# Optimization experiments

Measured on AMD Instinct MI355X. Metric: run time of the kernel, lower is better.

The kernel has to match this reference:

```python
import jax, jax.numpy as jnp
import numpy as np

B, T, D = 8, 2048, 128


def setup_inputs() -> dict:
    key = jax.random.key(0)
    kq, kk, kv = jax.random.split(key, 3)
    q = jax.random.normal(kq, (B, T, D), dtype=jnp.float32)
    k = jax.random.normal(kk, (B, T, D), dtype=jnp.float32)
    v = jax.random.normal(kv, (B, T, D), dtype=jnp.float32)
    # causal mask, broadcast over batch; 0 -> masked
    mask = jnp.tril(jnp.ones((T, T), dtype=jnp.int32))[None, :, :]
    mode = jnp.float32(0.5)  # learnable scalar parameter (init 0.5)
    return {"q": q, "k": k, "v": v, "mask": mask, "mode": mode}


def reference(q, k, v, mask, mode):
    scale = D ** (-0.5)
    # meson score: -(Q K^T) * scale
    meson = -jnp.einsum("btd,bsd->bts", q, k) * scale
    # baryon score: Q against K with feature dim rolled by 1
    k_perm = jnp.roll(k, shift=1, axis=-1)
    baryon = jnp.einsum("btd,bsd->bts", q, k_perm) * scale
    alpha = jax.nn.sigmoid(mode)
    attn = alpha * meson + (1.0 - alpha) * baryon
    attn = jnp.where(mask == 0, -jnp.inf, attn)
    attn = jax.nn.softmax(attn, axis=-1)
    return jnp.einsum("bts,bsd->btd", attn, v)
```

## Files before the change

### kernel.cpp

```cpp
#include <hip/hip_runtime.h>
#include <hip/hip_bf16.h>
#include <cstdint>
#include <cstddef>


typedef __attribute__((ext_vector_type(8))) short short8;
typedef __attribute__((ext_vector_type(4))) float f32x4;

#define T_DIM 2048
#define D_DIM 128
#define B_DIM 8
#define SEGT 4
#define POSLOTS_PER_B 56
#define MLSLOTS_PER_B 72

__device__ __forceinline__ unsigned short f2bf(float f) {
  unsigned u = __builtin_bit_cast(unsigned, f);
  u += 0x7FFFu + ((u >> 16) & 1u);
  return (unsigned short)(u >> 16);
}
__device__ __forceinline__ float bf2f(unsigned short u) {
  return __uint_as_float(((unsigned)u) << 16);
}
__device__ __forceinline__ void gload_lds16(const void* g, void* l) {
  __builtin_amdgcn_global_load_lds(
      (const __attribute__((address_space(1))) unsigned int*)g,
      (__attribute__((address_space(3))) unsigned int*)l, 16, 0, 0);
}

__global__ __launch_bounds__(256) void prep_all(
    const float* __restrict__ q, const float* __restrict__ k, const float* __restrict__ v,
    const float* __restrict__ modep,
    unsigned short* __restrict__ qbf, unsigned short* __restrict__ kbf,
    unsigned short* __restrict__ vt)
{
  __shared__ unsigned short tile[64 * 136];
  const int b = blockIdx.x, s0 = blockIdx.y * 64;
  const int tid = threadIdx.x;
  const float alpha = 1.f / (1.f + __expf(-modep[0]));
  const float scale = 0.08838834764831845f;
  const float ca = -alpha * scale, cb = (1.f - alpha) * scale;

#pragma unroll
  for (int u = 0; u < 4; ++u) {
    int c = u * 256 + tid;
    int r = c >> 4, c8 = c & 15;
    size_t row = (size_t)b * T_DIM + s0 + r;
    float4 ka = *(const float4*)(k + row * D_DIM + c8 * 8);
    float4 kb2 = *(const float4*)(k + row * D_DIM + c8 * 8 + 4);
    short8 ko = { (short)f2bf(ka.x), (short)f2bf(ka.y), (short)f2bf(ka.z), (short)f2bf(ka.w),
                  (short)f2bf(kb2.x), (short)f2bf(kb2.y), (short)f2bf(kb2.z), (short)f2bf(kb2.w) };
    *(short8*)(kbf + row * D_DIM + c8 * 8) = ko;
    const float* qr = q + row * D_DIM;
    float e[9];
    float4 f0 = *(const float4*)(qr + c8 * 8);
    float4 f1 = *(const float4*)(qr + c8 * 8 + 4);
    e[0] = f0.x; e[1] = f0.y; e[2] = f0.z; e[3] = f0.w;
    e[4] = f1.x; e[5] = f1.y; e[6] = f1.z; e[7] = f1.w;
    e[8] = qr[(c8 * 8 + 8) & 127];
    short8 qo;
#pragma unroll
    for (int j = 0; j < 8; ++j) qo[j] = (short)f2bf(ca * e[j] + cb * e[j + 1]);
    *(short8*)(qbf + row * D_DIM + c8 * 8) = qo;
    float4 va = *(const float4*)(v + row * D_DIM + c8 * 8);
    float4 vb2 = *(const float4*)(v + row * D_DIM + c8 * 8 + 4);
    short8 vo = { (short)f2bf(va.x), (short)f2bf(va.y), (short)f2bf(va.z), (short)f2bf(va.w),
                  (short)f2bf(vb2.x), (short)f2bf(vb2.y), (short)f2bf(vb2.z), (short)f2bf(vb2.w) };
    *(short8*)(tile + r * 136 + c8 * 8) = vo;
  }
  __syncthreads();
#pragma unroll
  for (int u = 0; u < 8; ++u) {
    int c = u * 256 + tid;
    int d = c >> 4, sq = c & 15;
    ushort4 o = { tile[(sq * 4 + 0) * 136 + d], tile[(sq * 4 + 1) * 136 + d],
                  tile[(sq * 4 + 2) * 136 + d], tile[(sq * 4 + 3) * 136 + d] };
    *(ushort4*)(vt + ((size_t)b * D_DIM + d) * T_DIM + s0 + sq * 4) = o;
  }
}

__global__ __launch_bounds__(256, 2) void attn_kernel(
    const unsigned short* __restrict__ qbf, const unsigned short* __restrict__ kbf,
    const unsigned short* __restrict__ vt, float* __restrict__ out,
    unsigned short* __restrict__ po, float* __restrict__ ml)
{
  __shared__ uint4 smem4[4608];
  char* smem = (char*)smem4;
  const int tid = threadIdx.x;
  const int w = tid >> 6, lane = tid & 63;
  const int t16 = lane & 15, g = lane >> 4;
  const int b = blockIdx.x;
  const int c = blockIdx.y;
  const int s = blockIdx.z;
  const int nt = 2 * c + 2;
  const int nseg = (c + 2) >> 1;
  if (s >= nseg) return;
  const int t0 = s * SEGT;
  const int t1 = min(nt, t0 + SEGT);
  const int qb = c * 128 + w * 32;

  char* pw = smem + 65536 + w * 2048;
  const unsigned short* kbase = kbf + (size_t)b * T_DIM * D_DIM;
  const unsigned short* vbase = vt + (size_t)b * D_DIM * T_DIM;

  short8 qf[2][4];
#pragma unroll
  for (int mt = 0; mt < 2; ++mt) {
    const unsigned short* qr = qbf + ((size_t)b * T_DIM + qb + mt * 16 + t16) * D_DIM + g * 8;
#pragma unroll
    for (int dd = 0; dd < 4; ++dd) qf[mt][dd] = *(const short8*)(qr + dd * 32);
  }

  f32x4 acc[2][8];
#pragma unroll
  for (int mt = 0; mt < 2; ++mt)
#pragma unroll
    for (int dt = 0; dt < 8; ++dt) acc[mt][dt] = (f32x4){0.f, 0.f, 0.f, 0.f};
  float mrun[2][4], lsum[2][4];
#pragma unroll
  for (int mt = 0; mt < 2; ++mt)
#pragma unroll
    for (int r = 0; r < 4; ++r) { mrun[mt][r] = -1e30f; lsum[mt][r] = 0.f; }

  auto stage = [&](int cur, int kt) {
    const int kv0 = kt * 64;
    char* kb = smem + cur * 16384;
    char* vb = smem + 32768 + cur * 16384;
#pragma unroll
    for (int u = 0; u < 4; ++u) {
      int s_loc = w * 16 + u * 4 + (lane >> 4);
      int slot = (lane & 15) ^ (s_loc & 7);
      gload_lds16(kbase + (size_t)(kv0 + s_loc) * D_DIM + slot * 8,
                  kb + w * 4096 + u * 1024);
    }
#pragma unroll
    for (int u = 0; u < 4; ++u) {
      int d_loc = w * 32 + u * 8 + (lane >> 3);
      int vslot = (lane & 7) ^ (d_loc & 7);
      gload_lds16(vbase + (size_t)d_loc * T_DIM + kv0 + vslot * 8,
                  vb + w * 4096 + u * 1024);
    }
  };

  stage(0, t0);
  __syncthreads();
  int cur = 0;

  for (int kt = t0; kt < t1; ++kt) {
    if (kt + 1 < t1) stage(cur ^ 1, kt + 1);
    const int kv0 = kt * 64;

    if (kv0 <= qb + 31) {
      char* kb = smem + cur * 16384;
      char* vb = smem + 32768 + cur * 16384;

      f32x4 sj[2][4];
#pragma unroll
      for (int jt = 0; jt < 4; ++jt) {
        int srow = jt * 16 + t16;
        int rb = srow * 256, swz = (srow & 7) << 4;
        f32x4 s0 = (f32x4){0.f, 0.f, 0.f, 0.f};
        f32x4 s1 = (f32x4){0.f, 0.f, 0.f, 0.f};
#pragma unroll
        for (int dd = 0; dd < 4; ++dd) {
          short8 kf = *(const short8*)(kb + ((rb + dd * 64 + g * 16) ^ swz));
          s0 = __builtin_amdgcn_mfma_f32_16x16x32_bf16(qf[0][dd], kf, s0, 0, 0, 0);
          s1 = __builtin_amdgcn_mfma_f32_16x16x32_bf16(qf[1][dd], kf, s1, 0, 0, 0);
        }
        sj[0][jt] = s0; sj[1][jt] = s1;
      }

      if (kv0 + 63 > qb) {
#pragma unroll
        for (int mt = 0; mt < 2; ++mt)
#pragma unroll
          for (int jt = 0; jt < 4; ++jt) {
            int sg = kv0 + jt * 16 + t16;
#pragma unroll
            for (int r = 0; r < 4; ++r) {
              int tg = qb + mt * 16 + 4 * g + r;
              if (sg > tg) sj[mt][jt][r] = -1e30f;
            }
          }
      }

      float lm[2][4];
      int ok = 1;
#pragma unroll
      for (int mt = 0; mt < 2; ++mt)
#pragma unroll
        for (int r = 0; r < 4; ++r) {
          lm[mt][r] = fmaxf(fmaxf(sj[mt][0][r], sj[mt][1][r]),
                            fmaxf(sj[mt][2][r], sj[mt][3][r]));
          ok &= (lm[mt][r] <= mrun[mt][r] + 8.0f);
        }
      if (!__all(ok)) {
#pragma unroll
        for (int mt = 0; mt < 2; ++mt) {
          float tm[4];
#pragma unroll
          for (int r = 0; r < 4; ++r) tm[r] = lm[mt][r];
#pragma unroll
          for (int r = 0; r < 4; ++r) {
            tm[r] = fmaxf(tm[r], __shfl_xor(tm[r], 1));
            tm[r] = fmaxf(tm[r], __shfl_xor(tm[r], 2));
            tm[r] = fmaxf(tm[r], __shfl_xor(tm[r], 4));
            tm[r] = fmaxf(tm[r], __shfl_xor(tm[r], 8));
          }
#pragma unroll
          for (int r = 0; r < 4; ++r) {
            float mnew = fmaxf(mrun[mt][r], tm[r]);
            float corr = __expf(mrun[mt][r] - mnew);
            mrun[mt][r] = mnew;
            lsum[mt][r] *= corr;
#pragma unroll
            for (int dt = 0; dt < 8; ++dt) acc[mt][dt][r] *= corr;
          }
        }
      }

#pragma unroll
      for (int mt = 0; mt < 2; ++mt) {
        float ls[4] = {0.f, 0.f, 0.f, 0.f};
#pragma unroll
        for (int jt = 0; jt < 4; ++jt)
#pragma unroll
          for (int r = 0; r < 4; ++r) {
            float p = __expf(sj[mt][jt][r] - mrun[mt][r]);
            sj[mt][jt][r] = p;
            ls[r] += p;
          }
#pragma unroll
        for (int r = 0; r < 4; ++r) lsum[mt][r] += ls[r];
#pragma unroll
        for (int jt = 0; jt < 4; ++jt)
#pragma unroll
          for (int r = 0; r < 4; ++r) {
            int rloc = 4 * g + r;
            *(unsigned short*)(pw + rloc * 128 + ((2 * (jt * 16 + t16)) ^ ((rloc & 7) << 4))) =
                f2bf(sj[mt][jt][r]);
          }
#pragma unroll
        for (int k0 = 0; k0 < 2; ++k0) {
          short8 pf = *(const short8*)(pw + t16 * 128 + ((k0 * 64 + g * 16) ^ ((t16 & 7) << 4)));
#pragma unroll
          for (int dt = 0; dt < 8; ++dt) {
            int d = dt * 16 + t16;
            short8 vf = *(const short8*)(vb + d * 128 + (((k0 * 4 + g) << 4) ^ ((d & 7) << 4)));
            acc[mt][dt] = __builtin_amdgcn_mfma_f32_16x16x32_bf16(pf, vf, acc[mt][dt], 0, 0, 0);
          }
        }
      }
    }

    __syncthreads();
    cur ^= 1;
  }

  float lred[2][4];
#pragma unroll
  for (int mt = 0; mt < 2; ++mt)
#pragma unroll
    for (int r = 0; r < 4; ++r) {
      float v0 = lsum[mt][r];
      v0 += __shfl_xor(v0, 1);
      v0 += __shfl_xor(v0, 2);
      v0 += __shfl_xor(v0, 4);
      v0 += __shfl_xor(v0, 8);
      lred[mt][r] = v0;
    }

  if (nseg == 1) {
#pragma unroll
    for (int mt = 0; mt < 2; ++mt)
#pragma unroll
      for (int r = 0; r < 4; ++r) {
        float inv = 1.0f / lred[mt][r];
#pragma unroll
        for (int dt = 0; dt < 8; ++dt)
          out[((size_t)b * T_DIM + qb + mt * 16 + 4 * g + r) * D_DIM + dt * 16 + t16] =
              acc[mt][dt][r] * inv;
      }
  } else {
    int pofs = 0;
    for (int cc = 0; cc < c; ++cc) pofs += ((cc + 2) >> 1) - 1;
    if (s == 0) {
#pragma unroll
      for (int mt = 0; mt < 2; ++mt)
#pragma unroll
        for (int r = 0; r < 4; ++r)
#pragma unroll
          for (int dt = 0; dt < 8; ++dt)
            out[((size_t)b * T_DIM + qb + mt * 16 + 4 * g + r) * D_DIM + dt * 16 + t16] =
                acc[mt][dt][r];
    } else {
      unsigned short* pob = po + ((size_t)b * POSLOTS_PER_B + pofs + (s - 1)) * 16384;
#pragma unroll
      for (int mt = 0; mt < 2; ++mt)
#pragma unroll
        for (int r = 0; r < 4; ++r) {
          int rb = w * 32 + mt * 16 + 4 * g + r;
#pragma unroll
          for (int dt = 0; dt < 8; ++dt)
            pob[rb * 128 + dt * 16 + t16] = f2bf(acc[mt][dt][r]);
        }
    }
    if (t16 == 0) {
      const size_t mlslot = (size_t)b * MLSLOTS_PER_B + pofs + c + s;
#pragma unroll
      for (int mt = 0; mt < 2; ++mt)
#pragma unroll
        for (int r = 0; r < 4; ++r) {
          int rb = w * 32 + mt * 16 + 4 * g + r;
          ml[mlslot * 256 + rb] = mrun[mt][r];
          ml[mlslot * 256 + 128 + rb] = lred[mt][r];
        }
    }
  }
}

__global__ __launch_bounds__(256) void combine_kernel(
    const unsigned short* __restrict__ po, const float* __restrict__ ml,
    float* __restrict__ out)
{
  const int tid = threadIdx.x;
  const int b = blockIdx.x;
  const int c = 2 + (int)blockIdx.y;
  const int nseg = (c + 2) >> 1;
  int pofs = 0;
  for (int cc = 0; cc < c; ++cc) pofs += ((cc + 2) >> 1) - 1;
  const size_t mlbase = (size_t)b * MLSLOTS_PER_B + pofs + c;
  const size_t pobase = (size_t)b * POSLOTS_PER_B + pofs;

  __shared__ float wgt[128][8];
  if (tid < 128) {
    float M = -1e30f;
    for (int s = 0; s < nseg; ++s)
      M = fmaxf(M, ml[(mlbase + s) * 256 + tid]);
    float L = 0.f;
    for (int s = 0; s < nseg; ++s) {
      float e = __expf(ml[(mlbase + s) * 256 + tid] - M);
      wgt[tid][s] = e;
      L += e * ml[(mlbase + s) * 256 + 128 + tid];
    }
    float invL = 1.f / L;
    for (int s = 0; s < nseg; ++s) wgt[tid][s] *= invL;
  }
  __syncthreads();

#pragma unroll
  for (int it = 0; it < 8; ++it) {
    int vid = it * 256 + tid;
    int r = vid >> 4, ch = vid & 15;
    float* op = out + ((size_t)b * T_DIM + c * 128 + r) * D_DIM + ch * 8;
    float4 a0 = *(const float4*)op;
    float4 a1 = *(const float4*)(op + 4);
    float w0 = wgt[r][0];
    float o[8] = { w0 * a0.x, w0 * a0.y, w0 * a0.z, w0 * a0.w,
                   w0 * a1.x, w0 * a1.y, w0 * a1.z, w0 * a1.w };
    for (int s = 1; s < nseg; ++s) {
      short8 pv = *(const short8*)(po + (pobase + s - 1) * 16384 + r * 128 + ch * 8);
      float ws = wgt[r][s];
#pragma unroll
      for (int j = 0; j < 8; ++j) o[j] += ws * bf2f((unsigned short)pv[j]);
    }
    *(float4*)op = (float4){o[0], o[1], o[2], o[3]};
    *(float4*)(op + 4) = (float4){o[4], o[5], o[6], o[7]};
  }
}

extern "C" void kernel_launch(void* const* d_in, const int* in_sizes, int n_in,
                              void* d_out, int out_size, void* d_ws, size_t ws_size,
                              hipStream_t stream) {
  const float* q = (const float*)d_in[0];
  const float* k = (const float*)d_in[1];
  const float* v = (const float*)d_in[2];
  const float* mode = (const float*)d_in[4];
  float* out = (float*)d_out;

  char* ws = (char*)d_ws;
  unsigned short* qbf = (unsigned short*)(ws);
  unsigned short* kbf = (unsigned short*)(ws + 4194304);
  unsigned short* vtb = (unsigned short*)(ws + 8388608);
  unsigned short* po  = (unsigned short*)(ws + 12582912);
  float*          ml  = (float*)(ws + 27262976);

  prep_all<<<dim3(B_DIM, T_DIM / 64), 256, 0, stream>>>(q, k, v, mode, qbf, kbf, vtb);
  attn_kernel<<<dim3(B_DIM, 16, 8), 256, 0, stream>>>(qbf, kbf, vtb, out, po, ml);
  combine_kernel<<<dim3(B_DIM, 14), 256, 0, stream>>>(po, ml, out);
}
```

Measured before the change: 61.61 us.

## Transpose MFMA operands so each lane owns a query row, fuse Q prep into attention

Swaps the MFMA A/B operands so score and output tiles are transposed, letting each lane hold one query row. Row max and sum then need only two cross-group shuffles instead of four, and output stores become vectorized float4 writes. Q bf16 conversion and the alpha/scale/roll mixing move into the attention kernel, removing the qbf buffer and its write and read. Softmax switches to exp2 with log2e folded into Q, and the rescale threshold rises from 8 to 11. In exchange, each wave's P scratch in LDS doubles, and Q preprocessing is repeated across the segment blocks of a chunk.

New measurement: 66.72 us. 8.3% more time.

```diff
diff --git a/kernel.cpp b/kernel.cpp
--- a/kernel.cpp
+++ b/kernel.cpp
@@ -13,6 +13,7 @@
 #define SEGT 4
 #define POSLOTS_PER_B 56
 #define MLSLOTS_PER_B 72
+#define LOG2E 1.4426950408889634f
 
 __device__ __forceinline__ unsigned short f2bf(float f) {
   unsigned u = __builtin_bit_cast(unsigned, f);
@@ -22,25 +23,22 @@
 __device__ __forceinline__ float bf2f(unsigned short u) {
   return __uint_as_float(((unsigned)u) << 16);
 }
+__device__ __forceinline__ unsigned pack2bf(float a, float b) {
+  return (unsigned)f2bf(a) | ((unsigned)f2bf(b) << 16);
+}
 __device__ __forceinline__ void gload_lds16(const void* g, void* l) {
   __builtin_amdgcn_global_load_lds(
       (const __attribute__((address_space(1))) unsigned int*)g,
       (__attribute__((address_space(3))) unsigned int*)l, 16, 0, 0);
 }
 
-__global__ __launch_bounds__(256) void prep_all(
-    const float* __restrict__ q, const float* __restrict__ k, const float* __restrict__ v,
-    const float* __restrict__ modep,
-    unsigned short* __restrict__ qbf, unsigned short* __restrict__ kbf,
-    unsigned short* __restrict__ vt)
+__global__ __launch_bounds__(256) void prep_kv(
+    const float* __restrict__ k, const float* __restrict__ v,
+    unsigned short* __restrict__ kbf, unsigned short* __restrict__ vt)
 {
   __shared__ unsigned short tile[64 * 136];
   const int b = blockIdx.x, s0 = blockIdx.y * 64;
   const int tid = threadIdx.x;
-  const float alpha = 1.f / (1.f + __expf(-modep[0]));
-  const float scale = 0.08838834764831845f;
-  const float ca = -alpha * scale, cb = (1.f - alpha) * scale;
-
 #pragma unroll
   for (int u = 0; u < 4; ++u) {
     int c = u * 256 + tid;
@@ -51,17 +49,6 @@
     short8 ko = { (short)f2bf(ka.x), (short)f2bf(ka.y), (short)f2bf(ka.z), (short)f2bf(ka.w),
                   (short)f2bf(kb2.x), (short)f2bf(kb2.y), (short)f2bf(kb2.z), (short)f2bf(kb2.w) };
     *(short8*)(kbf + row * D_DIM + c8 * 8) = ko;
-    const float* qr = q + row * D_DIM;
-    float e[9];
-    float4 f0 = *(const float4*)(qr + c8 * 8);
-    float4 f1 = *(const float4*)(qr + c8 * 8 + 4);
-    e[0] = f0.x; e[1] = f0.y; e[2] = f0.z; e[3] = f0.w;
-    e[4] = f1.x; e[5] = f1.y; e[6] = f1.z; e[7] = f1.w;
-    e[8] = qr[(c8 * 8 + 8) & 127];
-    short8 qo;
-#pragma unroll
-    for (int j = 0; j < 8; ++j) qo[j] = (short)f2bf(ca * e[j] + cb * e[j + 1]);
-    *(short8*)(qbf + row * D_DIM + c8 * 8) = qo;
     float4 va = *(const float4*)(v + row * D_DIM + c8 * 8);
     float4 vb2 = *(const float4*)(v + row * D_DIM + c8 * 8 + 4);
     short8 vo = { (short)f2bf(va.x), (short)f2bf(va.y), (short)f2bf(va.z), (short)f2bf(va.w),
@@ -80,11 +67,11 @@
 }
 
 __global__ __launch_bounds__(256, 2) void attn_kernel(
-    const unsigned short* __restrict__ qbf, const unsigned short* __restrict__ kbf,
-    const unsigned short* __restrict__ vt, float* __restrict__ out,
-    unsigned short* __restrict__ po, float* __restrict__ ml)
+    const float* __restrict__ q, const unsigned short* __restrict__ kbf,
+    const unsigned short* __restrict__ vt, const float* __restrict__ modep,
+    float* __restrict__ out, unsigned short* __restrict__ po, float* __restrict__ ml)
 {
-  __shared__ uint4 smem4[4608];
+  __shared__ uint4 smem4[5120];
   char* smem = (char*)smem4;
   const int tid = threadIdx.x;
   const int w = tid >> 6, lane = tid & 63;
@@ -99,16 +86,32 @@
   const int t1 = min(nt, t0 + SEGT);
   const int qb = c * 128 + w * 32;
 
-  char* pw = smem + 65536 + w * 2048;
+  char* pw = smem + 65536 + w * 4096;
+  const int px = 4 * (t16 & 7);
   const unsigned short* kbase = kbf + (size_t)b * T_DIM * D_DIM;
   const unsigned short* vbase = vt + (size_t)b * D_DIM * T_DIM;
 
+  const float alpha = 1.f / (1.f + __expf(-modep[0]));
+  const float scale = 0.08838834764831845f;
+  const float ca = -alpha * scale * LOG2E, cb = (1.f - alpha) * scale * LOG2E;
   short8 qf[2][4];
 #pragma unroll
   for (int mt = 0; mt < 2; ++mt) {
-    const unsigned short* qr = qbf + ((size_t)b * T_DIM + qb + mt * 16 + t16) * D_DIM + g * 8;
-#pragma unroll
-    for (int dd = 0; dd < 4; ++dd) qf[mt][dd] = *(const short8*)(qr + dd * 32);
+    const float* qr = q + ((size_t)b * T_DIM + qb + mt * 16 + t16) * D_DIM;
+#pragma unroll
+    for (int dd = 0; dd < 4; ++dd) {
+      int dstart = dd * 32 + g * 8;
+      float e[9];
+      float4 f0 = *(const float4*)(qr + dstart);
+      float4 f1 = *(const float4*)(qr + dstart + 4);
+      e[0] = f0.x; e[1] = f0.y; e[2] = f0.z; e[3] = f0.w;
+      e[4] = f1.x; e[5] = f1.y; e[6] = f1.z; e[7] = f1.w;
+      e[8] = qr[(dstart + 8) & 127];
+      short8 qv;
+#pragma unroll
+      for (int i = 0; i < 8; ++i) qv[i] = (short)f2bf(ca * e[i] + cb * e[i + 1]);
+      qf[mt][dd] = qv;
+    }
   }
 
   f32x4 acc[2][8];
@@ -116,11 +119,8 @@
   for (int mt = 0; mt < 2; ++mt)
 #pragma unroll
     for (int dt = 0; dt < 8; ++dt) acc[mt][dt] = (f32x4){0.f, 0.f, 0.f, 0.f};
-  float mrun[2][4], lsum[2][4];
-#pragma unroll
-  for (int mt = 0; mt < 2; ++mt)
-#pragma unroll
-    for (int r = 0; r < 4; ++r) { mrun[mt][r] = -1e30f; lsum[mt][r] = 0.f; }
+  float mrun[2] = {-1e30f, -1e30f};
+  float lsum[2] = {0.f, 0.f};
 
   auto stage = [&](int cur, int kt) {
     const int kv0 = kt * 64;
@@ -164,157 +164,149 @@
 #pragma unroll
         for (int dd = 0; dd < 4; ++dd) {
           short8 kf = *(const short8*)(kb + ((rb + dd * 64 + g * 16) ^ swz));
-          s0 = __builtin_amdgcn_mfma_f32_16x16x32_bf16(qf[0][dd], kf, s0, 0, 0, 0);
-          s1 = __builtin_amdgcn_mfma_f32_16x16x32_bf16(qf[1][dd], kf, s1, 0, 0, 0);
+          s0 = __builtin_amdgcn_mfma_f32_16x16x32_bf16(kf, qf[0][dd], s0, 0, 0, 0);
+          s1 = __builtin_amdgcn_mfma_f32_16x16x32_bf16(kf, qf[1][dd], s1, 0, 0, 0);
         }
         sj[0][jt] = s0; sj[1][jt] = s1;
       }
 
       if (kv0 + 63 > qb) {
 #pragma unroll
-        for (int mt = 0; mt < 2; ++mt)
-#pragma unroll
-          for (int jt = 0; jt < 4; ++jt) {
-            int sg = kv0 + jt * 16 + t16;
+        for (int mt = 0; mt < 2; ++mt) {
+          int tg = qb + mt * 16 + t16;
+#pragma unroll
+          for (int jt = 0; jt < 4; ++jt)
 #pragma unroll
             for (int r = 0; r < 4; ++r) {
-              int tg = qb + mt * 16 + 4 * g + r;
+              int sg = kv0 + jt * 16 + 4 * g + r;
               if (sg > tg) sj[mt][jt][r] = -1e30f;
             }
+        }
+      }
+
+      float lm[2];
+      int ok = 1;
+#pragma unroll
+      for (int mt = 0; mt < 2; ++mt) {
+        float m0 = fmaxf(fmaxf(sj[mt][0][0], sj[mt][0][1]), fmaxf(sj[mt][0][2], sj[mt][0][3]));
+        float m1 = fmaxf(fmaxf(sj[mt][1][0], sj[mt][1][1]), fmaxf(sj[mt][1][2], sj[mt][1][3]));
+        float m2 = fmaxf(fmaxf(sj[mt][2][0], sj[mt][2][1]), fmaxf(sj[mt][2][2], sj[mt][2][3]));
+        float m3 = fmaxf(fmaxf(sj[mt][3][0], sj[mt][3][1]), fmaxf(sj[mt][3][2], sj[mt][3][3]));
+        lm[mt] = fmaxf(fmaxf(m0, m1), fmaxf(m2, m3));
+        ok &= (lm[mt] <= mrun[mt] + 11.0f);
+      }
+      if (!__all(ok)) {
+#pragma unroll
+        for (int mt = 0; mt < 2; ++mt) {
+          float tm = lm[mt];
+          tm = fmaxf(tm, __shfl_xor(tm, 16));
+          tm = fmaxf(tm, __shfl_xor(tm, 32));
+          float mnew = fmaxf(mrun[mt], tm);
+          float corr = exp2f(mrun[mt] - mnew);
+          mrun[mt] = mnew;
+          lsum[mt] *= corr;
+#pragma unroll
+          for (int dt = 0; dt < 8; ++dt) acc[mt][dt] *= corr;
+        }
+      }
+
+#pragma unroll
+      for (int mt = 0; mt < 2; ++mt) {
+        float ls = 0.f;
+#pragma unroll
+        for (int jt = 0; jt < 4; ++jt)
+#pragma unroll
+          for (int r = 0; r < 4; ++r) {
+            float p = exp2f(sj[mt][jt][r] - mrun[mt]);
+            sj[mt][jt][r] = p;
+            ls += p;
           }
-      }
-
-      float lm[2][4];
-      int ok = 1;
+        lsum[mt] += ls;
+        char* pm = pw + mt * 2048;
+#pragma unroll
+        for (int jt = 0; jt < 4; ++jt) {
+          unsigned lo = pack2bf(sj[mt][jt][0], sj[mt][jt][1]);
+          unsigned hi = pack2bf(sj[mt][jt][2], sj[mt][jt][3]);
+          unsigned long long wd = (unsigned long long)lo | ((unsigned long long)hi << 32);
+          *(unsigned long long*)(pm + t16 * 128 + (((8 * jt + 2 * g) ^ px) << 2)) = wd;
+        }
+      }
+
+      short8 pf[2][2];
 #pragma unroll
       for (int mt = 0; mt < 2; ++mt)
 #pragma unroll
-        for (int r = 0; r < 4; ++r) {
-          lm[mt][r] = fmaxf(fmaxf(sj[mt][0][r], sj[mt][1][r]),
-                            fmaxf(sj[mt][2][r], sj[mt][3][r]));
-          ok &= (lm[mt][r] <= mrun[mt][r] + 8.0f);
-        }
-      if (!__all(ok)) {
-#pragma unroll
-        for (int mt = 0; mt < 2; ++mt) {
-          float tm[4];
-#pragma unroll
-          for (int r = 0; r < 4; ++r) tm[r] = lm[mt][r];
-#pragma unroll
-          for (int r = 0; r < 4; ++r) {
-            tm[r] = fmaxf(tm[r], __shfl_xor(tm[r], 1));
-            tm[r] = fmaxf(tm[r], __shfl_xor(tm[r], 2));
-            tm[r] = fmaxf(tm[r], __shfl_xor(tm[r], 4));
-            tm[r] = fmaxf(tm[r], __shfl_xor(tm[r], 8));
-          }
-#pragma unroll
-          for (int r = 0; r < 4; ++r) {
-            float mnew = fmaxf(mrun[mt][r], tm[r]);
-            float corr = __expf(mrun[mt][r] - mnew);
-            mrun[mt][r] = mnew;
-            lsum[mt][r] *= corr;
-#pragma unroll
-            for (int dt = 0; dt < 8; ++dt) acc[mt][dt][r] *= corr;
-          }
-        }
-      }
-
-#pragma unroll
-      for (int mt = 0; mt < 2; ++mt) {
-        float ls[4] = {0.f, 0.f, 0.f, 0.f};
-#pragma unroll
-        for (int jt = 0; jt < 4; ++jt)
-#pragma unroll
-          for (int r = 0; r < 4; ++r) {
-            float p = __expf(sj[mt][jt][r] - mrun[mt][r]);
-            sj[mt][jt][r] = p;
-            ls[r] += p;
-          }
-#pragma unroll
-        for (int r = 0; r < 4; ++r) lsum[mt][r] += ls[r];
-#pragma unroll
-        for (int jt = 0; jt < 4; ++jt)
-#pragma unroll
-          for (int r = 0; r < 4; ++r) {
-            int rloc = 4 * g + r;
-            *(unsigned short*)(pw + rloc * 128 + ((2 * (jt * 16 + t16)) ^ ((rloc & 7) << 4))) =
-                f2bf(sj[mt][jt][r]);
-          }
-#pragma unroll
-        for (int k0 = 0; k0 < 2; ++k0) {
-          short8 pf = *(const short8*)(pw + t16 * 128 + ((k0 * 64 + g * 16) ^ ((t16 & 7) << 4)));
-#pragma unroll
-          for (int dt = 0; dt < 8; ++dt) {
-            int d = dt * 16 + t16;
-            short8 vf = *(const short8*)(vb + d * 128 + (((k0 * 4 + g) << 4) ^ ((d & 7) << 4)));
-            acc[mt][dt] = __builtin_amdgcn_mfma_f32_16x16x32_bf16(pf, vf, acc[mt][dt], 0, 0, 0);
-          }
-        }
-      }
+        for (int k0 = 0; k0 < 2; ++k0)
+          pf[mt][k0] = *(const short8*)(pw + mt * 2048 + t16 * 128 +
+                                        (((16 * k0 + 4 * g) ^ px) << 2));
+
+#pragma unroll
+      for (int k0 = 0; k0 < 2; ++k0)
+#pragma unroll
+        for (int dt = 0; dt < 8; ++dt) {
+          int d = dt * 16 + t16;
+          short8 vf = *(const short8*)(vb + d * 128 + (((k0 * 4 + g) << 4) ^ ((d & 7) << 4)));
+          acc[0][dt] = __builtin_amdgcn_mfma_f32_16x16x32_bf16(vf, pf[0][k0], acc[0][dt], 0, 0, 0);
+          acc[1][dt] = __builtin_amdgcn_mfma_f32_16x16x32_bf16(vf, pf[1][k0], acc[1][dt], 0, 0, 0);
+        }
     }
 
     __syncthreads();
     cur ^= 1;
   }
 
-  float lred[2][4];
-#pragma unroll
-  for (int mt = 0; mt < 2; ++mt)
-#pragma unroll
-    for (int r = 0; r < 4; ++r) {
-      float v0 = lsum[mt][r];
-      v0 += __shfl_xor(v0, 1);
-      v0 += __shfl_xor(v0, 2);
-      v0 += __shfl_xor(v0, 4);
-      v0 += __shfl_xor(v0, 8);
-      lred[mt][r] = v0;
-    }
+  float lred[2];
+#pragma unroll
+  for (int mt = 0; mt < 2; ++mt) {
+    float v0 = lsum[mt];
+    v0 += __shfl_xor(v0, 16);
+    v0 += __shfl_xor(v0, 32);
+    lred[mt] = v0;
+  }
 
   if (nseg == 1) {
 #pragma unroll
-    for (int mt = 0; mt < 2; ++mt)
-#pragma unroll
-      for (int r = 0; r < 4; ++r) {
-        float inv = 1.0f / lred[mt][r];
-#pragma unroll
-        for (int dt = 0; dt < 8; ++dt)
-          out[((size_t)b * T_DIM + qb + mt * 16 + 4 * g + r) * D_DIM + dt * 16 + t16] =
-              acc[mt][dt][r] * inv;
-      }
+    for (int mt = 0; mt < 2; ++mt) {
+      float inv = 1.0f / lred[mt];
+      float* orow = out + ((size_t)b * T_DIM + qb + mt * 16 + t16) * D_DIM;
+#pragma unroll
+      for (int dt = 0; dt < 8; ++dt) {
+        f32x4 o = acc[mt][dt] * inv;
+        *(f32x4*)(orow + dt * 16 + 4 * g) = o;
+      }
+    }
   } else {
     int pofs = 0;
     for (int cc = 0; cc < c; ++cc) pofs += ((cc + 2) >> 1) - 1;
     if (s == 0) {
 #pragma unroll
-      for (int mt = 0; mt < 2; ++mt)
-#pragma unroll
-        for (int r = 0; r < 4; ++r)
-#pragma unroll
-          for (int dt = 0; dt < 8; ++dt)
-            out[((size_t)b * T_DIM + qb + mt * 16 + 4 * g + r) * D_DIM + dt * 16 + t16] =
-                acc[mt][dt][r];
+      for (int mt = 0; mt < 2; ++mt) {
+        float* orow = out + ((size_t)b * T_DIM + qb + mt * 16 + t16) * D_DIM;
+#pragma unroll
+        for (int dt = 0; dt < 8; ++dt)
+          *(f32x4*)(orow + dt * 16 + 4 * g) = acc[mt][dt];
+      }
     } else {
       unsigned short* pob = po + ((size_t)b * POSLOTS_PER_B + pofs + (s - 1)) * 16384;
 #pragma unroll
-      for (int mt = 0; mt < 2; ++mt)
-#pragma unroll
-        for (int r = 0; r < 4; ++r) {
-          int rb = w * 32 + mt * 16 + 4 * g + r;
-#pragma unroll
-          for (int dt = 0; dt < 8; ++dt)
-            pob[rb * 128 + dt * 16 + t16] = f2bf(acc[mt][dt][r]);
-        }
-    }
-    if (t16 == 0) {
+      for (int mt = 0; mt < 2; ++mt) {
+        unsigned short* prow = pob + (w * 32 + mt * 16 + t16) * 128;
+#pragma unroll
+        for (int dt = 0; dt < 8; ++dt) {
+          ushort4 o = { f2bf(acc[mt][dt][0]), f2bf(acc[mt][dt][1]),
+                        f2bf(acc[mt][dt][2]), f2bf(acc[mt][dt][3]) };
+          *(ushort4*)(prow + dt * 16 + 4 * g) = o;
+        }
+      }
+    }
+    if (g == 0) {
       const size_t mlslot = (size_t)b * MLSLOTS_PER_B + pofs + c + s;
 #pragma unroll
-      for (int mt = 0; mt < 2; ++mt)
-#pragma unroll
-        for (int r = 0; r < 4; ++r) {
-          int rb = w * 32 + mt * 16 + 4 * g + r;
-          ml[mlslot * 256 + rb] = mrun[mt][r];
-          ml[mlslot * 256 + 128 + rb] = lred[mt][r];
-        }
+      for (int mt = 0; mt < 2; ++mt) {
+        int rb = w * 32 + mt * 16 + t16;
+        ml[mlslot * 256 + rb] = mrun[mt];
+        ml[mlslot * 256 + 128 + rb] = lred[mt];
+      }
     }
   }
 }
@@ -339,7 +331,7 @@
       M = fmaxf(M, ml[(mlbase + s) * 256 + tid]);
     float L = 0.f;
     for (int s = 0; s < nseg; ++s) {
-      float e = __expf(ml[(mlbase + s) * 256 + tid] - M);
+      float e = exp2f(ml[(mlbase + s) * 256 + tid] - M);
       wgt[tid][s] = e;
       L += e * ml[(mlbase + s) * 256 + 128 + tid];
     }
@@ -379,13 +371,12 @@
   float* out = (float*)d_out;
 
   char* ws = (char*)d_ws;
-  unsigned short* qbf = (unsigned short*)(ws);
-  unsigned short* kbf = (unsigned short*)(ws + 4194304);
-  unsigned short* vtb = (unsigned short*)(ws + 8388608);
-  unsigned short* po  = (unsigned short*)(ws + 12582912);
-  float*          ml  = (float*)(ws + 27262976);
-
-  prep_all<<<dim3(B_DIM, T_DIM / 64), 256, 0, stream>>>(q, k, v, mode, qbf, kbf, vtb);
-  attn_kernel<<<dim3(B_DIM, 16, 8), 256, 0, stream>>>(qbf, kbf, vtb, out, po, ml);
+  unsigned short* kbf = (unsigned short*)(ws);
+  unsigned short* vtb = (unsigned short*)(ws + 4194304);
+  unsigned short* po  = (unsigned short*)(ws + 8388608);
+  float*          ml  = (float*)(ws + 23068672);
+
+  prep_kv<<<dim3(B_DIM, T_DIM / 64), 256, 0, stream>>>(k, v, kbf, vtb);
+  attn_kernel<<<dim3(B_DIM, 16, 8), 256, 0, stream>>>(q, kbf, vtb, mode, out, po, ml);
   combine_kernel<<<dim3(B_DIM, 14), 256, 0, stream>>>(po, ml, out);
 }
```

## Shrink attention tiles to 32x32 with more KV segments and exp2 softmax

Applied to the files above, without the earlier changes.

Reworks the attention kernel from 128-query-row blocks of four waves with double-buffered 64-wide KV tiles into 32-query-row blocks of two waves with single-buffered 32-wide KV tiles. Blocks are launched in reverse causal order, and KV is split into segments of 8 tiles, with partial outputs merged in the combine kernel. The log2(e) factor is folded into the prep-stage Q scaling so the softmax can use exp2f. The goal is better causal load balance and occupancy through many small blocks, at the cost of less K/V reuse per block, more global traffic, two barriers per tile and lost load/compute overlap.

Result: faster. 53.20 us, median of 2 (-13.7%).

```diff
diff --git a/kernel.cpp b/kernel.cpp
--- a/kernel.cpp
+++ b/kernel.cpp
@@ -10,9 +10,10 @@
 #define T_DIM 2048
 #define D_DIM 128
 #define B_DIM 8
-#define SEGT 4
-#define POSLOTS_PER_B 56
-#define MLSLOTS_PER_B 72
+#define SEGT 8
+#define POSLOTS_PER_B 224
+#define MLSLOTS_PER_B 288
+#define LOG2E 1.4426950408889634f
 
 __device__ __forceinline__ unsigned short f2bf(float f) {
   unsigned u = __builtin_bit_cast(unsigned, f);
@@ -39,7 +40,7 @@
   const int tid = threadIdx.x;
   const float alpha = 1.f / (1.f + __expf(-modep[0]));
   const float scale = 0.08838834764831845f;
-  const float ca = -alpha * scale, cb = (1.f - alpha) * scale;
+  const float ca = -alpha * scale * LOG2E, cb = (1.f - alpha) * scale * LOG2E;
 
 #pragma unroll
   for (int u = 0; u < 4; ++u) {
@@ -79,53 +80,48 @@
   }
 }
 
-__global__ __launch_bounds__(256, 2) void attn_kernel(
+__global__ __launch_bounds__(128, 4) void attn_kernel(
     const unsigned short* __restrict__ qbf, const unsigned short* __restrict__ kbf,
     const unsigned short* __restrict__ vt, float* __restrict__ out,
     unsigned short* __restrict__ po, float* __restrict__ ml)
 {
-  __shared__ uint4 smem4[4608];
+  __shared__ uint4 smem4[1152];
   char* smem = (char*)smem4;
   const int tid = threadIdx.x;
   const int w = tid >> 6, lane = tid & 63;
   const int t16 = lane & 15, g = lane >> 4;
   const int b = blockIdx.x;
-  const int c = blockIdx.y;
+  const int c = 63 - (int)blockIdx.y;
   const int s = blockIdx.z;
-  const int nt = 2 * c + 2;
-  const int nseg = (c + 2) >> 1;
+  const int nt = c + 1;
+  const int nseg = (nt + SEGT - 1) >> 3;
   if (s >= nseg) return;
   const int t0 = s * SEGT;
   const int t1 = min(nt, t0 + SEGT);
-  const int qb = c * 128 + w * 32;
-
-  char* pw = smem + 65536 + w * 2048;
+  const int qb16 = c * 32 + w * 16;
+
+  char* kb = smem;
+  char* vb = smem + 8192;
+  char* pw = smem + 16384 + w * 1024;
   const unsigned short* kbase = kbf + (size_t)b * T_DIM * D_DIM;
   const unsigned short* vbase = vt + (size_t)b * D_DIM * T_DIM;
 
-  short8 qf[2][4];
-#pragma unroll
-  for (int mt = 0; mt < 2; ++mt) {
-    const unsigned short* qr = qbf + ((size_t)b * T_DIM + qb + mt * 16 + t16) * D_DIM + g * 8;
-#pragma unroll
-    for (int dd = 0; dd < 4; ++dd) qf[mt][dd] = *(const short8*)(qr + dd * 32);
-  }
-
-  f32x4 acc[2][8];
-#pragma unroll
-  for (int mt = 0; mt < 2; ++mt)
-#pragma unroll
-    for (int dt = 0; dt < 8; ++dt) acc[mt][dt] = (f32x4){0.f, 0.f, 0.f, 0.f};
-  float mrun[2][4], lsum[2][4];
-#pragma unroll
-  for (int mt = 0; mt < 2; ++mt)
-#pragma unroll
-    for (int r = 0; r < 4; ++r) { mrun[mt][r] = -1e30f; lsum[mt][r] = 0.f; }
-
-  auto stage = [&](int cur, int kt) {
-    const int kv0 = kt * 64;
-    char* kb = smem + cur * 16384;
-    char* vb = smem + 32768 + cur * 16384;
+  short8 qf[4];
+  {
+    const unsigned short* qr = qbf + ((size_t)b * T_DIM + qb16 + t16) * D_DIM + g * 8;
+#pragma unroll
+    for (int dd = 0; dd < 4; ++dd) qf[dd] = *(const short8*)(qr + dd * 32);
+  }
+
+  f32x4 acc[8];
+#pragma unroll
+  for (int dt = 0; dt < 8; ++dt) acc[dt] = (f32x4){0.f, 0.f, 0.f, 0.f};
+  float mrun[4] = {-1e30f, -1e30f, -1e30f, -1e30f};
+  float lsum[4] = {0.f, 0.f, 0.f, 0.f};
+
+  for (int kt = t0; kt < t1; ++kt) {
+    const int kv0 = kt * 32;
+    __syncthreads();
 #pragma unroll
     for (int u = 0; u < 4; ++u) {
       int s_loc = w * 16 + u * 4 + (lane >> 4);
@@ -135,186 +131,128 @@
     }
 #pragma unroll
     for (int u = 0; u < 4; ++u) {
-      int d_loc = w * 32 + u * 8 + (lane >> 3);
-      int vslot = (lane & 7) ^ (d_loc & 7);
+      int d_loc = w * 64 + u * 16 + (lane >> 2);
+      int vslot = (lane & 3) ^ (d_loc & 3);
       gload_lds16(vbase + (size_t)d_loc * T_DIM + kv0 + vslot * 8,
                   vb + w * 4096 + u * 1024);
     }
-  };
-
-  stage(0, t0);
-  __syncthreads();
-  int cur = 0;
-
-  for (int kt = t0; kt < t1; ++kt) {
-    if (kt + 1 < t1) stage(cur ^ 1, kt + 1);
-    const int kv0 = kt * 64;
-
-    if (kv0 <= qb + 31) {
-      char* kb = smem + cur * 16384;
-      char* vb = smem + 32768 + cur * 16384;
-
-      f32x4 sj[2][4];
-#pragma unroll
-      for (int jt = 0; jt < 4; ++jt) {
-        int srow = jt * 16 + t16;
-        int rb = srow * 256, swz = (srow & 7) << 4;
-        f32x4 s0 = (f32x4){0.f, 0.f, 0.f, 0.f};
-        f32x4 s1 = (f32x4){0.f, 0.f, 0.f, 0.f};
-#pragma unroll
-        for (int dd = 0; dd < 4; ++dd) {
-          short8 kf = *(const short8*)(kb + ((rb + dd * 64 + g * 16) ^ swz));
-          s0 = __builtin_amdgcn_mfma_f32_16x16x32_bf16(qf[0][dd], kf, s0, 0, 0, 0);
-          s1 = __builtin_amdgcn_mfma_f32_16x16x32_bf16(qf[1][dd], kf, s1, 0, 0, 0);
+    __syncthreads();
+
+    f32x4 sj[2];
+#pragma unroll
+    for (int jt = 0; jt < 2; ++jt) {
+      int srow = jt * 16 + t16;
+      int rb = srow * 256, swz = (srow & 7) << 4;
+      f32x4 sc = (f32x4){0.f, 0.f, 0.f, 0.f};
+#pragma unroll
+      for (int dd = 0; dd < 4; ++dd) {
+        short8 kf = *(const short8*)(kb + ((rb + dd * 64 + g * 16) ^ swz));
+        sc = __builtin_amdgcn_mfma_f32_16x16x32_bf16(qf[dd], kf, sc, 0, 0, 0);
+      }
+      sj[jt] = sc;
+    }
+
+    if (kt == c) {
+#pragma unroll
+      for (int jt = 0; jt < 2; ++jt) {
+        int sg = kv0 + jt * 16 + t16;
+#pragma unroll
+        for (int r = 0; r < 4; ++r) {
+          int tg = qb16 + 4 * g + r;
+          if (sg > tg) sj[jt][r] = -1e30f;
         }
-        sj[0][jt] = s0; sj[1][jt] = s1;
-      }
-
-      if (kv0 + 63 > qb) {
-#pragma unroll
-        for (int mt = 0; mt < 2; ++mt)
-#pragma unroll
-          for (int jt = 0; jt < 4; ++jt) {
-            int sg = kv0 + jt * 16 + t16;
-#pragma unroll
-            for (int r = 0; r < 4; ++r) {
-              int tg = qb + mt * 16 + 4 * g + r;
-              if (sg > tg) sj[mt][jt][r] = -1e30f;
-            }
-          }
-      }
-
-      float lm[2][4];
-      int ok = 1;
-#pragma unroll
-      for (int mt = 0; mt < 2; ++mt)
-#pragma unroll
-        for (int r = 0; r < 4; ++r) {
-          lm[mt][r] = fmaxf(fmaxf(sj[mt][0][r], sj[mt][1][r]),
-                            fmaxf(sj[mt][2][r], sj[mt][3][r]));
-          ok &= (lm[mt][r] <= mrun[mt][r] + 8.0f);
-        }
-      if (!__all(ok)) {
-#pragma unroll
-        for (int mt = 0; mt < 2; ++mt) {
-          float tm[4];
-#pragma unroll
-          for (int r = 0; r < 4; ++r) tm[r] = lm[mt][r];
-#pragma unroll
-          for (int r = 0; r < 4; ++r) {
-            tm[r] = fmaxf(tm[r], __shfl_xor(tm[r], 1));
-            tm[r] = fmaxf(tm[r], __shfl_xor(tm[r], 2));
-            tm[r] = fmaxf(tm[r], __shfl_xor(tm[r], 4));
-            tm[r] = fmaxf(tm[r], __shfl_xor(tm[r], 8));
-          }
-#pragma unroll
-          for (int r = 0; r < 4; ++r) {
-            float mnew = fmaxf(mrun[mt][r], tm[r]);
-            float corr = __expf(mrun[mt][r] - mnew);
-            mrun[mt][r] = mnew;
-            lsum[mt][r] *= corr;
-#pragma unroll
-            for (int dt = 0; dt < 8; ++dt) acc[mt][dt][r] *= corr;
-          }
-        }
-      }
-
-#pragma unroll
-      for (int mt = 0; mt < 2; ++mt) {
-        float ls[4] = {0.f, 0.f, 0.f, 0.f};
-#pragma unroll
-        for (int jt = 0; jt < 4; ++jt)
-#pragma unroll
-          for (int r = 0; r < 4; ++r) {
-            float p = __expf(sj[mt][jt][r] - mrun[mt][r]);
-            sj[mt][jt][r] = p;
-            ls[r] += p;
-          }
-#pragma unroll
-        for (int r = 0; r < 4; ++r) lsum[mt][r] += ls[r];
-#pragma unroll
-        for (int jt = 0; jt < 4; ++jt)
-#pragma unroll
-          for (int r = 0; r < 4; ++r) {
-            int rloc = 4 * g + r;
-            *(unsigned short*)(pw + rloc * 128 + ((2 * (jt * 16 + t16)) ^ ((rloc & 7) << 4))) =
-                f2bf(sj[mt][jt][r]);
-          }
-#pragma unroll
-        for (int k0 = 0; k0 < 2; ++k0) {
-          short8 pf = *(const short8*)(pw + t16 * 128 + ((k0 * 64 + g * 16) ^ ((t16 & 7) << 4)));
-#pragma unroll
-          for (int dt = 0; dt < 8; ++dt) {
-            int d = dt * 16 + t16;
-            short8 vf = *(const short8*)(vb + d * 128 + (((k0 * 4 + g) << 4) ^ ((d & 7) << 4)));
-            acc[mt][dt] = __builtin_amdgcn_mfma_f32_16x16x32_bf16(pf, vf, acc[mt][dt], 0, 0, 0);
-          }
-        }
-      }
-    }
-
-    __syncthreads();
-    cur ^= 1;
-  }
-
-  float lred[2][4];
-#pragma unroll
-  for (int mt = 0; mt < 2; ++mt)
+      }
+    }
+
+    float lm[4];
+    int ok = 1;
 #pragma unroll
     for (int r = 0; r < 4; ++r) {
-      float v0 = lsum[mt][r];
-      v0 += __shfl_xor(v0, 1);
-      v0 += __shfl_xor(v0, 2);
-      v0 += __shfl_xor(v0, 4);
-      v0 += __shfl_xor(v0, 8);
-      lred[mt][r] = v0;
-    }
+      lm[r] = fmaxf(sj[0][r], sj[1][r]);
+      ok &= (lm[r] <= mrun[r] + 11.0f);
+    }
+    if (!__all(ok)) {
+#pragma unroll
+      for (int r = 0; r < 4; ++r) {
+        float tm = lm[r];
+        tm = fmaxf(tm, __shfl_xor(tm, 1));
+        tm = fmaxf(tm, __shfl_xor(tm, 2));
+        tm = fmaxf(tm, __shfl_xor(tm, 4));
+        tm = fmaxf(tm, __shfl_xor(tm, 8));
+        float mnew = fmaxf(mrun[r], tm);
+        float corr = exp2f(mrun[r] - mnew);
+        mrun[r] = mnew;
+        lsum[r] *= corr;
+#pragma unroll
+        for (int dt = 0; dt < 8; ++dt) acc[dt][r] *= corr;
+      }
+    }
+
+#pragma unroll
+    for (int jt = 0; jt < 2; ++jt)
+#pragma unroll
+      for (int r = 0; r < 4; ++r) {
+        float p = exp2f(sj[jt][r] - mrun[r]);
+        lsum[r] += p;
+        int row = 4 * g + r;
+        *(unsigned short*)(pw + row * 64 + ((jt * 32 + t16 * 2) ^ ((row >> 2) << 4))) = f2bf(p);
+      }
+
+    short8 pf = *(const short8*)(pw + t16 * 64 + ((g * 16) ^ ((t16 >> 2) << 4)));
+#pragma unroll
+    for (int dt = 0; dt < 8; ++dt) {
+      int d = dt * 16 + t16;
+      short8 vf = *(const short8*)(vb + d * 64 + ((g * 16) ^ ((d & 3) << 4)));
+      acc[dt] = __builtin_amdgcn_mfma_f32_16x16x32_bf16(pf, vf, acc[dt], 0, 0, 0);
+    }
+  }
+
+  float lred[4];
+#pragma unroll
+  for (int r = 0; r < 4; ++r) {
+    float v0 = lsum[r];
+    v0 += __shfl_xor(v0, 1);
+    v0 += __shfl_xor(v0, 2);
+    v0 += __shfl_xor(v0, 4);
+    v0 += __shfl_xor(v0, 8);
+    lred[r] = v0;
+  }
 
   if (nseg == 1) {
 #pragma unroll
-    for (int mt = 0; mt < 2; ++mt)
-#pragma unroll
-      for (int r = 0; r < 4; ++r) {
-        float inv = 1.0f / lred[mt][r];
-#pragma unroll
-        for (int dt = 0; dt < 8; ++dt)
-          out[((size_t)b * T_DIM + qb + mt * 16 + 4 * g + r) * D_DIM + dt * 16 + t16] =
-              acc[mt][dt][r] * inv;
-      }
+    for (int r = 0; r < 4; ++r) {
+      float inv = 1.0f / lred[r];
+#pragma unroll
+      for (int dt = 0; dt < 8; ++dt)
+        out[((size_t)b * T_DIM + qb16 + 4 * g + r) * D_DIM + dt * 16 + t16] = acc[dt][r] * inv;
+    }
   } else {
     int pofs = 0;
-    for (int cc = 0; cc < c; ++cc) pofs += ((cc + 2) >> 1) - 1;
+    for (int cc = 0; cc < c; ++cc) pofs += ((cc + SEGT) >> 3) - 1;
     if (s == 0) {
 #pragma unroll
-      for (int mt = 0; mt < 2; ++mt)
-#pragma unroll
-        for (int r = 0; r < 4; ++r)
-#pragma unroll
-          for (int dt = 0; dt < 8; ++dt)
-            out[((size_t)b * T_DIM + qb + mt * 16 + 4 * g + r) * D_DIM + dt * 16 + t16] =
-                acc[mt][dt][r];
+      for (int r = 0; r < 4; ++r)
+#pragma unroll
+        for (int dt = 0; dt < 8; ++dt)
+          out[((size_t)b * T_DIM + qb16 + 4 * g + r) * D_DIM + dt * 16 + t16] = acc[dt][r];
     } else {
-      unsigned short* pob = po + ((size_t)b * POSLOTS_PER_B + pofs + (s - 1)) * 16384;
-#pragma unroll
-      for (int mt = 0; mt < 2; ++mt)
-#pragma unroll
-        for (int r = 0; r < 4; ++r) {
-          int rb = w * 32 + mt * 16 + 4 * g + r;
-#pragma unroll
-          for (int dt = 0; dt < 8; ++dt)
-            pob[rb * 128 + dt * 16 + t16] = f2bf(acc[mt][dt][r]);
-        }
+      unsigned short* pob = po + ((size_t)b * POSLOTS_PER_B + pofs + (s - 1)) * 4096;
+#pragma unroll
+      for (int r = 0; r < 4; ++r) {
+        int rb = w * 16 + 4 * g + r;
+#pragma unroll
+        for (int dt = 0; dt < 8; ++dt)
+          pob[rb * 128 + dt * 16 + t16] = f2bf(acc[dt][r]);
+      }
     }
     if (t16 == 0) {
       const size_t mlslot = (size_t)b * MLSLOTS_PER_B + pofs + c + s;
 #pragma unroll
-      for (int mt = 0; mt < 2; ++mt)
-#pragma unroll
-        for (int r = 0; r < 4; ++r) {
-          int rb = w * 32 + mt * 16 + 4 * g + r;
-          ml[mlslot * 256 + rb] = mrun[mt][r];
-          ml[mlslot * 256 + 128 + rb] = lred[mt][r];
-        }
+      for (int r = 0; r < 4; ++r) {
+        int rb = w * 16 + 4 * g + r;
+        ml[mlslot * 64 + rb] = mrun[r];
+        ml[mlslot * 64 + 32 + rb] = lred[r];
+      }
     }
   }
 }
@@ -325,23 +263,24 @@
 {
   const int tid = threadIdx.x;
   const int b = blockIdx.x;
-  const int c = 2 + (int)blockIdx.y;
-  const int nseg = (c + 2) >> 1;
+  const int c = SEGT + (int)blockIdx.y;
+  const int nt = c + 1;
+  const int nseg = (nt + SEGT - 1) >> 3;
   int pofs = 0;
-  for (int cc = 0; cc < c; ++cc) pofs += ((cc + 2) >> 1) - 1;
+  for (int cc = 0; cc < c; ++cc) pofs += ((cc + SEGT) >> 3) - 1;
   const size_t mlbase = (size_t)b * MLSLOTS_PER_B + pofs + c;
   const size_t pobase = (size_t)b * POSLOTS_PER_B + pofs;
 
-  __shared__ float wgt[128][8];
-  if (tid < 128) {
+  __shared__ float wgt[32][8];
+  if (tid < 32) {
     float M = -1e30f;
     for (int s = 0; s < nseg; ++s)
-      M = fmaxf(M, ml[(mlbase + s) * 256 + tid]);
+      M = fmaxf(M, ml[(mlbase + s) * 64 + tid]);
     float L = 0.f;
     for (int s = 0; s < nseg; ++s) {
-      float e = __expf(ml[(mlbase + s) * 256 + tid] - M);
+      float e = exp2f(ml[(mlbase + s) * 64 + tid] - M);
       wgt[tid][s] = e;
-      L += e * ml[(mlbase + s) * 256 + 128 + tid];
+      L += e * ml[(mlbase + s) * 64 + 32 + tid];
     }
     float invL = 1.f / L;
     for (int s = 0; s < nseg; ++s) wgt[tid][s] *= invL;
@@ -349,17 +288,17 @@
   __syncthreads();
 
 #pragma unroll
-  for (int it = 0; it < 8; ++it) {
+  for (int it = 0; it < 2; ++it) {
     int vid = it * 256 + tid;
     int r = vid >> 4, ch = vid & 15;
-    float* op = out + ((size_t)b * T_DIM + c * 128 + r) * D_DIM + ch * 8;
+    float* op = out + ((size_t)b * T_DIM + c * 32 + r) * D_DIM + ch * 8;
     float4 a0 = *(const float4*)op;
     float4 a1 = *(const float4*)(op + 4);
     float w0 = wgt[r][0];
     float o[8] = { w0 * a0.x, w0 * a0.y, w0 * a0.z, w0 * a0.w,
                    w0 * a1.x, w0 * a1.y, w0 * a1.z, w0 * a1.w };
     for (int s = 1; s < nseg; ++s) {
-      short8 pv = *(const short8*)(po + (pobase + s - 1) * 16384 + r * 128 + ch * 8);
+      short8 pv = *(const short8*)(po + (pobase + s - 1) * 4096 + r * 128 + ch * 8);
       float ws = wgt[r][s];
 #pragma unroll
       for (int j = 0; j < 8; ++j) o[j] += ws * bf2f((unsigned short)pv[j]);
@@ -386,6 +325,6 @@
   float*          ml  = (float*)(ws + 27262976);
 
   prep_all<<<dim3(B_DIM, T_DIM / 64), 256, 0, stream>>>(q, k, v, mode, qbf, kbf, vtb);
-  attn_kernel<<<dim3(B_DIM, 16, 8), 256, 0, stream>>>(qbf, kbf, vtb, out, po, ml);
-  combine_kernel<<<dim3(B_DIM, 14), 256, 0, stream>>>(po, ml, out);
-}
+  attn_kernel<<<dim3(B_DIM, 64, SEGT), 128, 0, stream>>>(qbf, kbf, vtb, out, po, ml);
+  combine_kernel<<<dim3(B_DIM, 64 - SEGT), 256, 0, stream>>>(po, ml, out);
+}
```
